# Performance work log

Hardware: AMD Instinct MI355X
Metric: run time of the kernel (lower is better)

Reference implementation:

```python
import jax, jax.numpy as jnp
import numpy as np


def setup_inputs() -> dict:
    key = jax.random.key(0)
    ks = jax.random.split(key, 6)
    B, S, T, E, D = 16, 128, 128, 512, 512  # batch, enc steps, dec steps, enc units, dec units
    scale = 0.05
    return {
        "enc": jax.random.normal(ks[0], (B, S, E), dtype=jnp.float32),
        "dec": jax.random.normal(ks[1], (B, T, D), dtype=jnp.float32),
        "W1": jax.random.normal(ks[2], (E, E), dtype=jnp.float32) * scale,
        "W2": jax.random.normal(ks[3], (D, E), dtype=jnp.float32) * scale,
        "b": jax.random.normal(ks[4], (1, 1, E), dtype=jnp.float32) * scale,
        "V": jax.random.normal(ks[5], (E, 1), dtype=jnp.float32) * scale,
    }


def reference(enc, dec, W1, W2, b, V):
    # Vectorized Bahdanau additive attention (the original loops over decoder
    # timesteps with keras.backend.rnn; the steps are independent so we batch them).
    W1_hs = jnp.einsum('bse,ef->bsf', enc, W1)            # [B,S,E] (computed once, not per step)
    W2_ht = jnp.einsum('btd,de->bte', dec, W2)            # [B,T,E]
    # tanh(W1.hs + W2.ht + b): broadcast to [B,T,S,E]
    scores = jnp.tanh(W1_hs[:, None, :, :] + W2_ht[:, :, None, :] + b)
    logits = jnp.einsum('btse,e->bts', scores, V[:, 0])   # [B,T,S]
    attn_weights = jax.nn.softmax(logits, axis=-1)        # softmax over encoder steps
    context_vectors = jnp.einsum('bts,bse->bte', attn_weights, enc)  # [B,T,E]
    return (context_vectors, attn_weights)
```

## Files before the change

### kernel.cpp

```cpp
#include <hip/hip_runtime.h>
#include <hip/hip_bf16.h>
#include <cstddef>


constexpr int nBt = 16, nSq = 128, nTq = 128, nEd = 512;

typedef __attribute__((ext_vector_type(4))) float f32x4;
typedef __attribute__((ext_vector_type(8))) short s16x8;

#define PRESCALE 2.8853900817779268f
#define LOG2E 1.4426950408889634f

__device__ __forceinline__ unsigned short to_bf(float f) {
    unsigned u = __builtin_bit_cast(unsigned, f);
    return (unsigned short)((u + 0x7FFFu + ((u >> 16) & 1u)) >> 16);
}
__device__ __forceinline__ float from_bf(unsigned short h) {
    unsigned u = ((unsigned)h) << 16;
    return __builtin_bit_cast(float, u);
}

__global__ __launch_bounds__(256) void kWprep(
    const float* __restrict__ W1, const float* __restrict__ W2,
    unsigned short* __restrict__ WT)
{
    const int z = blockIdx.z;
    const float* W = z ? W2 : W1;
    __shared__ float tl[32][33];
    const int r  = threadIdx.x >> 3;
    const int c4 = (threadIdx.x & 7) * 4;
    const int kB = blockIdx.y * 32;
    const int nB = blockIdx.x * 32;
    const float4 v = *(const float4*)&W[(size_t)(kB + r) * nEd + nB + c4];
    tl[r][c4 + 0] = v.x; tl[r][c4 + 1] = v.y;
    tl[r][c4 + 2] = v.z; tl[r][c4 + 3] = v.w;
    __syncthreads();
    unsigned short hh[4], ll[4];
    #pragma unroll
    for (int i = 0; i < 4; ++i) {
        const float x = tl[c4 + i][r];
        hh[i] = to_bf(x);
        ll[i] = to_bf(x - from_bf(hh[i]));
    }
    const size_t o = ((size_t)z * nEd + nB + r) * nEd + kB + c4;
    *(ushort4*)&WT[o] = *(ushort4*)hh;
    *(ushort4*)&WT[(size_t)2 * nEd * nEd + o] = *(ushort4*)ll;
}

__global__ __launch_bounds__(256) void kMgemm(
    const float* __restrict__ A0, const float* __restrict__ A1,
    const unsigned short* __restrict__ WT, const float* __restrict__ bias,
    float* __restrict__ C0, float* __restrict__ C1)
{
    const int z = blockIdx.z;
    const float* __restrict__ A = z ? A1 : A0;
    const unsigned short* __restrict__ Wh = WT + (size_t)z * nEd * nEd;
    const unsigned short* __restrict__ Wl = Wh + (size_t)2 * nEd * nEd;
    float* __restrict__ C = z ? C1 : C0;

    __shared__ unsigned short sAh[64][72];
    __shared__ unsigned short sAl[64][72];
    __shared__ unsigned short sBh[64][72];
    __shared__ unsigned short sBl[64][72];

    const int tid  = threadIdx.x;
    const int lane = tid & 63;
    const int wv   = tid >> 6;
    const int wm = (wv >> 1) * 32;
    const int wn = (wv & 1) * 32;
    const int rowB = blockIdx.y * 64;
    const int colB = blockIdx.x * 64;

    const int ar = tid >> 2, ak = (tid & 3) * 16;
    const int wr = tid >> 2, wk = (tid & 3) * 16;

    f32x4 acc[2][2] = {};
    const int l15 = lane & 15;
    const int kh  = lane >> 4;

    for (int k0 = 0; k0 < nEd; k0 += 64) {
        float4 ga[4];
        #pragma unroll
        for (int j = 0; j < 4; ++j)
            ga[j] = *(const float4*)&A[(size_t)(rowB + ar) * nEd + k0 + ak + 4 * j];
        const size_t wo = (size_t)(colB + wr) * nEd + k0 + wk;
        const s16x8 gh0 = *(const s16x8*)&Wh[wo];
        const s16x8 gh1 = *(const s16x8*)&Wh[wo + 8];
        const s16x8 gl0 = *(const s16x8*)&Wl[wo];
        const s16x8 gl1 = *(const s16x8*)&Wl[wo + 8];

        __syncthreads();
        #pragma unroll
        for (int j = 0; j < 4; ++j) {
            const float a4[4] = {ga[j].x, ga[j].y, ga[j].z, ga[j].w};
            unsigned short h[4], l[4];
            #pragma unroll
            for (int i = 0; i < 4; ++i) {
                h[i] = to_bf(a4[i]);
                l[i] = to_bf(a4[i] - from_bf(h[i]));
            }
            *(ushort4*)&sAh[ar][ak + 4 * j] = *(ushort4*)h;
            *(ushort4*)&sAl[ar][ak + 4 * j] = *(ushort4*)l;
        }
        *(s16x8*)&sBh[wr][wk]     = gh0;
        *(s16x8*)&sBh[wr][wk + 8] = gh1;
        *(s16x8*)&sBl[wr][wk]     = gl0;
        *(s16x8*)&sBl[wr][wk + 8] = gl1;
        __syncthreads();

        #pragma unroll
        for (int kk = 0; kk < 2; ++kk) {
            s16x8 fAh[2], fAl[2], fBh[2], fBl[2];
            #pragma unroll
            for (int mi = 0; mi < 2; ++mi) {
                fAh[mi] = *(const s16x8*)&sAh[wm + mi * 16 + l15][kk * 32 + kh * 8];
                fAl[mi] = *(const s16x8*)&sAl[wm + mi * 16 + l15][kk * 32 + kh * 8];
            }
            #pragma unroll
            for (int ni = 0; ni < 2; ++ni) {
                fBh[ni] = *(const s16x8*)&sBh[wn + ni * 16 + l15][kk * 32 + kh * 8];
                fBl[ni] = *(const s16x8*)&sBl[wn + ni * 16 + l15][kk * 32 + kh * 8];
            }
            #pragma unroll
            for (int mi = 0; mi < 2; ++mi)
                #pragma unroll
                for (int ni = 0; ni < 2; ++ni) {
                    f32x4 a = acc[mi][ni];
                    a = __builtin_amdgcn_mfma_f32_16x16x32_bf16(fAh[mi], fBh[ni], a, 0, 0, 0);
                    a = __builtin_amdgcn_mfma_f32_16x16x32_bf16(fAl[mi], fBh[ni], a, 0, 0, 0);
                    a = __builtin_amdgcn_mfma_f32_16x16x32_bf16(fAh[mi], fBl[ni], a, 0, 0, 0);
                    acc[mi][ni] = a;
                }
        }
    }

    #pragma unroll
    for (int ni = 0; ni < 2; ++ni) {
        const int col = colB + wn + ni * 16 + l15;
        const float bval = z ? bias[col] : 0.0f;
        #pragma unroll
        for (int mi = 0; mi < 2; ++mi) {
            #pragma unroll
            for (int r = 0; r < 4; ++r) {
                const int row = rowB + wm + mi * 16 + kh * 4 + r;
                C[(size_t)row * nEd + col] =
                    __builtin_amdgcn_exp2f((acc[mi][ni][r] + bval) * PRESCALE);
            }
        }
    }
}

__global__ __launch_bounds__(256) void kLogits(
    const float* __restrict__ X1e,
    const float* __restrict__ X2e,
    const float* __restrict__ V,
    float* __restrict__ lg)
{
    const int sg = blockIdx.x, tg = blockIdx.y, b = blockIdx.z;
    const int tid  = threadIdx.x;
    const int lane = tid & 63;
    const int w    = tid >> 6;
    const int s0 = sg * 32 + w * 8;
    const int t0 = tg * 4;

    const float4* vp = (const float4*)V;
    const float4  v0 = vp[lane * 2], v1 = vp[lane * 2 + 1];
    const float4 n0 = make_float4(-2.f * v0.x, -2.f * v0.y, -2.f * v0.z, -2.f * v0.w);
    const float4 n1 = make_float4(-2.f * v1.x, -2.f * v1.y, -2.f * v1.z, -2.f * v1.w);
    const float vsum = v0.x + v0.y + v0.z + v0.w + v1.x + v1.y + v1.z + v1.w;

    float4 c0[4], c1[4];
    #pragma unroll
    for (int i = 0; i < 4; ++i) {
        const float4* xp = (const float4*)(X2e + ((size_t)b * nTq + t0 + i) * nEd);
        c0[i] = xp[lane * 2];
        c1[i] = xp[lane * 2 + 1];
    }

    for (int si = 0; si < 8; ++si) {
        const int s = s0 + si;
        const float4* ap = (const float4*)(X1e + ((size_t)b * nSq + s) * nEd);
        const float4 x0 = ap[lane * 2], x1 = ap[lane * 2 + 1];
        float acc[4];
        #pragma unroll
        for (int t = 0; t < 4; ++t) {
            float a = vsum;
            a += n0.x * __builtin_amdgcn_rcpf(x0.x * c0[t].x + 1.0f);
            a += n0.y * __builtin_amdgcn_rcpf(x0.y * c0[t].y + 1.0f);
            a += n0.z * __builtin_amdgcn_rcpf(x0.z * c0[t].z + 1.0f);
            a += n0.w * __builtin_amdgcn_rcpf(x0.w * c0[t].w + 1.0f);
            a += n1.x * __builtin_amdgcn_rcpf(x1.x * c1[t].x + 1.0f);
            a += n1.y * __builtin_amdgcn_rcpf(x1.y * c1[t].y + 1.0f);
            a += n1.z * __builtin_amdgcn_rcpf(x1.z * c1[t].z + 1.0f);
            a += n1.w * __builtin_amdgcn_rcpf(x1.w * c1[t].w + 1.0f);
            acc[t] = a;
        }
        #pragma unroll
        for (int t = 0; t < 4; ++t) {
            float a = acc[t];
            #pragma unroll
            for (int off = 32; off >= 1; off >>= 1)
                a += __shfl_xor(a, off);
            if (lane == 0)
                lg[((size_t)b * nTq + t0 + t) * nSq + s] = a;
        }
    }
}

__global__ __launch_bounds__(256) void kEncT(
    const float* __restrict__ enc, unsigned short* __restrict__ encT)
{
    const int b = blockIdx.z;
    __shared__ float tl[32][33];
    const int r  = threadIdx.x >> 3;
    const int c4 = (threadIdx.x & 7) * 4;
    const int sB = blockIdx.y * 32;
    const int eB = blockIdx.x * 32;
    const float4 v = *(const float4*)&enc[((size_t)b * nSq + sB + r) * nEd + eB + c4];
    tl[r][c4 + 0] = v.x; tl[r][c4 + 1] = v.y;
    tl[r][c4 + 2] = v.z; tl[r][c4 + 3] = v.w;
    __syncthreads();
    unsigned short o[4];
    #pragma unroll
    for (int i = 0; i < 4; ++i) o[i] = to_bf(tl[c4 + i][r]);
    *(ushort4*)&encT[((size_t)b * nEd + eB + r) * nSq + sB + c4] = *(ushort4*)o;
}

__global__ __launch_bounds__(256) void kSoft(
    float* __restrict__ attnw,
    unsigned short* __restrict__ attnbf)
{
    const int bt = blockIdx.x * 4 + (threadIdx.x >> 6);
    const int lane = threadIdx.x & 63;
    const float l0 = attnw[(size_t)bt * nSq + lane];
    const float l1 = attnw[(size_t)bt * nSq + lane + 64];
    float m = fmaxf(l0, l1);
    #pragma unroll
    for (int off = 32; off >= 1; off >>= 1)
        m = fmaxf(m, __shfl_xor(m, off));
    const float e0 = __builtin_amdgcn_exp2f((l0 - m) * LOG2E);
    const float e1 = __builtin_amdgcn_exp2f((l1 - m) * LOG2E);
    float sum = e0 + e1;
    #pragma unroll
    for (int off = 32; off >= 1; off >>= 1)
        sum += __shfl_xor(sum, off);
    const float inv = __builtin_amdgcn_rcpf(sum);
    const float w0 = e0 * inv, w1 = e1 * inv;
    attnw[(size_t)bt * nSq + lane]      = w0;
    attnw[(size_t)bt * nSq + lane + 64] = w1;
    attnbf[(size_t)bt * nSq + lane]      = to_bf(w0);
    attnbf[(size_t)bt * nSq + lane + 64] = to_bf(w1);
}

__global__ __launch_bounds__(256) void kCtxMM(
    const unsigned short* __restrict__ attnbf,
    const unsigned short* __restrict__ encT,
    float* __restrict__ ctx)
{
    const int b  = blockIdx.z;
    const int tB = blockIdx.y * 32;
    const int eB = blockIdx.x * 64;

    __shared__ unsigned short sA[32][136];
    __shared__ unsigned short sB[64][136];

    const int tid  = threadIdx.x;
    const int lane = tid & 63;
    const int w    = tid >> 6;
    const int wm = (w >> 1) * 16;
    const int wn = (w & 1) * 32;
    const int l15 = lane & 15;
    const int kh  = lane >> 4;

    {
        const int r = tid >> 3, c = (tid & 7) * 16;
        const size_t o = ((size_t)b * nTq + tB + r) * nSq + c;
        *(s16x8*)&sA[r][c]     = *(const s16x8*)&attnbf[o];
        *(s16x8*)&sA[r][c + 8] = *(const s16x8*)&attnbf[o + 8];
    }
    {
        const int r = tid >> 2, c = (tid & 3) * 32;
        const size_t o = ((size_t)b * nEd + eB + r) * nSq + c;
        *(s16x8*)&sB[r][c]      = *(const s16x8*)&encT[o];
        *(s16x8*)&sB[r][c + 8]  = *(const s16x8*)&encT[o + 8];
        *(s16x8*)&sB[r][c + 16] = *(const s16x8*)&encT[o + 16];
        *(s16x8*)&sB[r][c + 24] = *(const s16x8*)&encT[o + 24];
    }
    __syncthreads();

    f32x4 acc[2] = {};
    #pragma unroll
    for (int kk = 0; kk < 4; ++kk) {
        const s16x8 fA = *(const s16x8*)&sA[wm + l15][kk * 32 + kh * 8];
        #pragma unroll
        for (int ni = 0; ni < 2; ++ni) {
            const s16x8 fB = *(const s16x8*)&sB[wn + ni * 16 + l15][kk * 32 + kh * 8];
            acc[ni] = __builtin_amdgcn_mfma_f32_16x16x32_bf16(fA, fB, acc[ni], 0, 0, 0);
        }
    }

    #pragma unroll
    for (int ni = 0; ni < 2; ++ni) {
        const int e = eB + wn + ni * 16 + l15;
        #pragma unroll
        for (int r = 0; r < 4; ++r) {
            const int t = tB + wm + kh * 4 + r;
            ctx[((size_t)b * nTq + t) * nEd + e] = acc[ni][r];
        }
    }
}

extern "C" void kernel_launch(void* const* d_in, const int* in_sizes, int n_in,
                              void* d_out, int out_size, void* d_ws, size_t ws_size,
                              hipStream_t stream) {
    const float* enc = (const float*)d_in[0];
    const float* dec = (const float*)d_in[1];
    const float* W1  = (const float*)d_in[2];
    const float* W2  = (const float*)d_in[3];
    const float* bv  = (const float*)d_in[4];
    const float* V   = (const float*)d_in[5];

    float* ctx   = (float*)d_out;
    float* attnw = (float*)d_out + (size_t)nBt * nTq * nEd;

    unsigned short* WT = (unsigned short*)d_out;

    float* ws0 = (float*)d_ws;
    float* ws1 = ws0 + (size_t)nBt * nSq * nEd;
    unsigned short* encT   = (unsigned short*)d_ws;
    unsigned short* attnbf = (unsigned short*)((char*)d_ws + 2*1024*1024);

    kWprep<<<dim3(nEd / 32, nEd / 32, 2), dim3(256), 0, stream>>>(W1, W2, WT);
    kMgemm<<<dim3(nEd / 64, (nBt * nSq) / 64, 2), dim3(256), 0, stream>>>(
        enc, dec, WT, bv, ws0, ws1);
    kLogits<<<dim3(4, 32, nBt), dim3(256), 0, stream>>>(ws0, ws1, V, attnw);
    kEncT<<<dim3(nEd / 32, nSq / 32, nBt), dim3(256), 0, stream>>>(enc, encT);
    kSoft<<<dim3((nBt * nTq) / 4), dim3(256), 0, stream>>>(attnw, attnbf);
    kCtxMM<<<dim3(nEd / 64, nTq / 32, nBt), dim3(256), 0, stream>>>(
        attnbf, encT, ctx);
}
```

Measured before the change: 59.40 us.

## Fuse logits with softmax, retile projection GEMM, convert attention weights in ctx GEMM

Result: slower. 84.76 us (+42.7%).

```diff
diff --git a/kernel.cpp b/kernel.cpp
--- a/kernel.cpp
+++ b/kernel.cpp
@@ -47,7 +47,7 @@
     *(ushort4*)&WT[(size_t)2 * nEd * nEd + o] = *(ushort4*)ll;
 }
 
-__global__ __launch_bounds__(256) void kMgemm(
+__global__ __launch_bounds__(256) void kMgemmB(
     const float* __restrict__ A0, const float* __restrict__ A1,
     const unsigned short* __restrict__ WT, const float* __restrict__ bias,
     float* __restrict__ C0, float* __restrict__ C1)
@@ -58,54 +58,55 @@
     const unsigned short* __restrict__ Wl = Wh + (size_t)2 * nEd * nEd;
     float* __restrict__ C = z ? C1 : C0;
 
-    __shared__ unsigned short sAh[64][72];
-    __shared__ unsigned short sAl[64][72];
-    __shared__ unsigned short sBh[64][72];
-    __shared__ unsigned short sBl[64][72];
+    __shared__ unsigned short sAh[32][72];
+    __shared__ unsigned short sAl[32][72];
+    __shared__ unsigned short sBh[128][72];
+    __shared__ unsigned short sBl[128][72];
 
     const int tid  = threadIdx.x;
     const int lane = tid & 63;
     const int wv   = tid >> 6;
-    const int wm = (wv >> 1) * 32;
-    const int wn = (wv & 1) * 32;
-    const int rowB = blockIdx.y * 64;
-    const int colB = blockIdx.x * 64;
-
-    const int ar = tid >> 2, ak = (tid & 3) * 16;
-    const int wr = tid >> 2, wk = (tid & 3) * 16;
+    const int rowB = blockIdx.y * 32;
+    const int colB = blockIdx.x * 128;
+
+    const int ar = tid >> 3, ak = (tid & 7) * 8;
+    const int br = tid >> 1, bc = (tid & 1) * 32;
 
     f32x4 acc[2][2] = {};
     const int l15 = lane & 15;
     const int kh  = lane >> 4;
 
     for (int k0 = 0; k0 < nEd; k0 += 64) {
-        float4 ga[4];
-        #pragma unroll
-        for (int j = 0; j < 4; ++j)
-            ga[j] = *(const float4*)&A[(size_t)(rowB + ar) * nEd + k0 + ak + 4 * j];
-        const size_t wo = (size_t)(colB + wr) * nEd + k0 + wk;
-        const s16x8 gh0 = *(const s16x8*)&Wh[wo];
-        const s16x8 gh1 = *(const s16x8*)&Wh[wo + 8];
-        const s16x8 gl0 = *(const s16x8*)&Wl[wo];
-        const s16x8 gl1 = *(const s16x8*)&Wl[wo + 8];
+        const float4 ga0 = *(const float4*)&A[(size_t)(rowB + ar) * nEd + k0 + ak];
+        const float4 ga1 = *(const float4*)&A[(size_t)(rowB + ar) * nEd + k0 + ak + 4];
+        const size_t wo = (size_t)(colB + br) * nEd + k0 + bc;
+        s16x8 gh[4], gl[4];
+        #pragma unroll
+        for (int j = 0; j < 4; ++j) {
+            gh[j] = *(const s16x8*)&Wh[wo + 8 * j];
+            gl[j] = *(const s16x8*)&Wl[wo + 8 * j];
+        }
 
         __syncthreads();
+        {
+            const float a8[8] = {ga0.x, ga0.y, ga0.z, ga0.w,
+                                 ga1.x, ga1.y, ga1.z, ga1.w};
+            unsigned short h[8], l[8];
+            #pragma unroll
+            for (int i = 0; i < 8; ++i) {
+                h[i] = to_bf(a8[i]);
+                l[i] = to_bf(a8[i] - from_bf(h[i]));
+            }
+            *(ushort4*)&sAh[ar][ak]     = *(ushort4*)&h[0];
+            *(ushort4*)&sAh[ar][ak + 4] = *(ushort4*)&h[4];
+            *(ushort4*)&sAl[ar][ak]     = *(ushort4*)&l[0];
+            *(ushort4*)&sAl[ar][ak + 4] = *(ushort4*)&l[4];
+        }
         #pragma unroll
         for (int j = 0; j < 4; ++j) {
-            const float a4[4] = {ga[j].x, ga[j].y, ga[j].z, ga[j].w};
-            unsigned short h[4], l[4];
-            #pragma unroll
-            for (int i = 0; i < 4; ++i) {
-                h[i] = to_bf(a4[i]);
-                l[i] = to_bf(a4[i] - from_bf(h[i]));
-            }
-            *(ushort4*)&sAh[ar][ak + 4 * j] = *(ushort4*)h;
-            *(ushort4*)&sAl[ar][ak + 4 * j] = *(ushort4*)l;
-        }
-        *(s16x8*)&sBh[wr][wk]     = gh0;
-        *(s16x8*)&sBh[wr][wk + 8] = gh1;
-        *(s16x8*)&sBl[wr][wk]     = gl0;
-        *(s16x8*)&sBl[wr][wk + 8] = gl1;
+            *(s16x8*)&sBh[br][bc + 8 * j] = gh[j];
+            *(s16x8*)&sBl[br][bc + 8 * j] = gl[j];
+        }
         __syncthreads();
 
         #pragma unroll
@@ -113,13 +114,13 @@
             s16x8 fAh[2], fAl[2], fBh[2], fBl[2];
             #pragma unroll
             for (int mi = 0; mi < 2; ++mi) {
-                fAh[mi] = *(const s16x8*)&sAh[wm + mi * 16 + l15][kk * 32 + kh * 8];
-                fAl[mi] = *(const s16x8*)&sAl[wm + mi * 16 + l15][kk * 32 + kh * 8];
+                fAh[mi] = *(const s16x8*)&sAh[mi * 16 + l15][kk * 32 + kh * 8];
+                fAl[mi] = *(const s16x8*)&sAl[mi * 16 + l15][kk * 32 + kh * 8];
             }
             #pragma unroll
             for (int ni = 0; ni < 2; ++ni) {
-                fBh[ni] = *(const s16x8*)&sBh[wn + ni * 16 + l15][kk * 32 + kh * 8];
-                fBl[ni] = *(const s16x8*)&sBl[wn + ni * 16 + l15][kk * 32 + kh * 8];
+                fBh[ni] = *(const s16x8*)&sBh[wv * 32 + ni * 16 + l15][kk * 32 + kh * 8];
+                fBl[ni] = *(const s16x8*)&sBl[wv * 32 + ni * 16 + l15][kk * 32 + kh * 8];
             }
             #pragma unroll
             for (int mi = 0; mi < 2; ++mi)
@@ -136,13 +137,13 @@
 
     #pragma unroll
     for (int ni = 0; ni < 2; ++ni) {
-        const int col = colB + wn + ni * 16 + l15;
+        const int col = colB + wv * 32 + ni * 16 + l15;
         const float bval = z ? bias[col] : 0.0f;
         #pragma unroll
         for (int mi = 0; mi < 2; ++mi) {
             #pragma unroll
             for (int r = 0; r < 4; ++r) {
-                const int row = rowB + wm + mi * 16 + kh * 4 + r;
+                const int row = rowB + mi * 16 + kh * 4 + r;
                 C[(size_t)row * nEd + col] =
                     __builtin_amdgcn_exp2f((acc[mi][ni][r] + bval) * PRESCALE);
             }
@@ -150,60 +151,97 @@
     }
 }
 
-__global__ __launch_bounds__(256) void kLogits(
+__global__ __launch_bounds__(256) void kLogSoft(
     const float* __restrict__ X1e,
     const float* __restrict__ X2e,
     const float* __restrict__ V,
-    float* __restrict__ lg)
-{
-    const int sg = blockIdx.x, tg = blockIdx.y, b = blockIdx.z;
+    float* __restrict__ attnw)
+{
+    const int tg = blockIdx.x, b = blockIdx.y;
     const int tid  = threadIdx.x;
     const int lane = tid & 63;
     const int w    = tid >> 6;
-    const int s0 = sg * 32 + w * 8;
     const int t0 = tg * 4;
 
-    const float4* vp = (const float4*)V;
-    const float4  v0 = vp[lane * 2], v1 = vp[lane * 2 + 1];
-    const float4 n0 = make_float4(-2.f * v0.x, -2.f * v0.y, -2.f * v0.z, -2.f * v0.w);
-    const float4 n1 = make_float4(-2.f * v1.x, -2.f * v1.y, -2.f * v1.z, -2.f * v1.w);
-    const float vsum = v0.x + v0.y + v0.z + v0.w + v1.x + v1.y + v1.z + v1.w;
-
-    float4 c0[4], c1[4];
-    #pragma unroll
-    for (int i = 0; i < 4; ++i) {
-        const float4* xp = (const float4*)(X2e + ((size_t)b * nTq + t0 + i) * nEd);
-        c0[i] = xp[lane * 2];
-        c1[i] = xp[lane * 2 + 1];
-    }
-
-    for (int si = 0; si < 8; ++si) {
-        const int s = s0 + si;
-        const float4* ap = (const float4*)(X1e + ((size_t)b * nSq + s) * nEd);
-        const float4 x0 = ap[lane * 2], x1 = ap[lane * 2 + 1];
-        float acc[4];
-        #pragma unroll
-        for (int t = 0; t < 4; ++t) {
-            float a = vsum;
-            a += n0.x * __builtin_amdgcn_rcpf(x0.x * c0[t].x + 1.0f);
-            a += n0.y * __builtin_amdgcn_rcpf(x0.y * c0[t].y + 1.0f);
-            a += n0.z * __builtin_amdgcn_rcpf(x0.z * c0[t].z + 1.0f);
-            a += n0.w * __builtin_amdgcn_rcpf(x0.w * c0[t].w + 1.0f);
-            a += n1.x * __builtin_amdgcn_rcpf(x1.x * c1[t].x + 1.0f);
-            a += n1.y * __builtin_amdgcn_rcpf(x1.y * c1[t].y + 1.0f);
-            a += n1.z * __builtin_amdgcn_rcpf(x1.z * c1[t].z + 1.0f);
-            a += n1.w * __builtin_amdgcn_rcpf(x1.w * c1[t].w + 1.0f);
-            acc[t] = a;
-        }
-        #pragma unroll
-        for (int t = 0; t < 4; ++t) {
-            float a = acc[t];
-            #pragma unroll
-            for (int off = 32; off >= 1; off >>= 1)
-                a += __shfl_xor(a, off);
-            if (lane == 0)
-                lg[((size_t)b * nTq + t0 + t) * nSq + s] = a;
-        }
+    __shared__ float x1t[128][68];
+    __shared__ float x2t[4][64];
+    __shared__ float nvt[64];
+    __shared__ float sm[4][nSq];
+
+    const int sr = 64 * (w & 1) + lane;
+    const int tp = (w >> 1) * 2;
+    const int srow = tid >> 1;
+    const int scol = (tid & 1) * 32;
+
+    const float* X1b = X1e + (size_t)b * nSq * nEd;
+    float acc0 = 0.f, acc1 = 0.f;
+
+    float4 pf[8];
+    #pragma unroll
+    for (int j = 0; j < 8; ++j)
+        pf[j] = *(const float4*)&X1b[(size_t)srow * nEd + scol + 4 * j];
+
+    for (int c = 0; c < 8; ++c) {
+        const int e0 = c * 64;
+        __syncthreads();
+        #pragma unroll
+        for (int j = 0; j < 8; ++j)
+            *(float4*)&x1t[srow][scol + 4 * j] = pf[j];
+        if (tid < 64) {
+            const int tt = tid >> 4, ee = (tid & 15) * 4;
+            *(float4*)&x2t[tt][ee] =
+                *(const float4*)&X2e[((size_t)b * nTq + t0 + tt) * nEd + e0 + ee];
+        } else if (tid < 80) {
+            const int ee = (tid - 64) * 4;
+            const float4 v = *(const float4*)&V[e0 + ee];
+            nvt[ee + 0] = -2.f * v.x; nvt[ee + 1] = -2.f * v.y;
+            nvt[ee + 2] = -2.f * v.z; nvt[ee + 3] = -2.f * v.w;
+        }
+        __syncthreads();
+
+        if (c < 7) {
+            #pragma unroll
+            for (int j = 0; j < 8; ++j)
+                pf[j] = *(const float4*)&X1b[(size_t)srow * nEd + e0 + 64 + scol + 4 * j];
+        }
+
+        #pragma unroll 4
+        for (int e4 = 0; e4 < 64; e4 += 4) {
+            const float4 x1v = *(const float4*)&x1t[sr][e4];
+            const float4 xa  = *(const float4*)&x2t[tp][e4];
+            const float4 xb  = *(const float4*)&x2t[tp + 1][e4];
+            const float4 nv  = *(const float4*)&nvt[e4];
+            acc0 += nv.x * __builtin_amdgcn_rcpf(x1v.x * xa.x + 1.0f);
+            acc1 += nv.x * __builtin_amdgcn_rcpf(x1v.x * xb.x + 1.0f);
+            acc0 += nv.y * __builtin_amdgcn_rcpf(x1v.y * xa.y + 1.0f);
+            acc1 += nv.y * __builtin_amdgcn_rcpf(x1v.y * xb.y + 1.0f);
+            acc0 += nv.z * __builtin_amdgcn_rcpf(x1v.z * xa.z + 1.0f);
+            acc1 += nv.z * __builtin_amdgcn_rcpf(x1v.z * xb.z + 1.0f);
+            acc0 += nv.w * __builtin_amdgcn_rcpf(x1v.w * xa.w + 1.0f);
+            acc1 += nv.w * __builtin_amdgcn_rcpf(x1v.w * xb.w + 1.0f);
+        }
+    }
+
+    sm[tp + 0][sr] = acc0;
+    sm[tp + 1][sr] = acc1;
+    __syncthreads();
+
+    {
+        const float l0 = sm[w][lane], l1 = sm[w][lane + 64];
+        float m = fmaxf(l0, l1);
+        #pragma unroll
+        for (int off = 32; off >= 1; off >>= 1)
+            m = fmaxf(m, __shfl_xor(m, off));
+        const float e0 = __builtin_amdgcn_exp2f((l0 - m) * LOG2E);
+        const float e1 = __builtin_amdgcn_exp2f((l1 - m) * LOG2E);
+        float sum = e0 + e1;
+        #pragma unroll
+        for (int off = 32; off >= 1; off >>= 1)
+            sum += __shfl_xor(sum, off);
+        const float inv = __builtin_amdgcn_rcpf(sum);
+        float* ap = attnw + ((size_t)b * nTq + t0 + w) * nSq;
+        ap[lane]      = e0 * inv;
+        ap[lane + 64] = e1 * inv;
     }
 }
 
@@ -226,34 +264,8 @@
     *(ushort4*)&encT[((size_t)b * nEd + eB + r) * nSq + sB + c4] = *(ushort4*)o;
 }
 
-__global__ __launch_bounds__(256) void kSoft(
-    float* __restrict__ attnw,
-    unsigned short* __restrict__ attnbf)
-{
-    const int bt = blockIdx.x * 4 + (threadIdx.x >> 6);
-    const int lane = threadIdx.x & 63;
-    const float l0 = attnw[(size_t)bt * nSq + lane];
-    const float l1 = attnw[(size_t)bt * nSq + lane + 64];
-    float m = fmaxf(l0, l1);
-    #pragma unroll
-    for (int off = 32; off >= 1; off >>= 1)
-        m = fmaxf(m, __shfl_xor(m, off));
-    const float e0 = __builtin_amdgcn_exp2f((l0 - m) * LOG2E);
-    const float e1 = __builtin_amdgcn_exp2f((l1 - m) * LOG2E);
-    float sum = e0 + e1;
-    #pragma unroll
-    for (int off = 32; off >= 1; off >>= 1)
-        sum += __shfl_xor(sum, off);
-    const float inv = __builtin_amdgcn_rcpf(sum);
-    const float w0 = e0 * inv, w1 = e1 * inv;
-    attnw[(size_t)bt * nSq + lane]      = w0;
-    attnw[(size_t)bt * nSq + lane + 64] = w1;
-    attnbf[(size_t)bt * nSq + lane]      = to_bf(w0);
-    attnbf[(size_t)bt * nSq + lane + 64] = to_bf(w1);
-}
-
 __global__ __launch_bounds__(256) void kCtxMM(
-    const unsigned short* __restrict__ attnbf,
+    const float* __restrict__ attnw,
     const unsigned short* __restrict__ encT,
     float* __restrict__ ctx)
 {
@@ -274,9 +286,16 @@
 
     {
         const int r = tid >> 3, c = (tid & 7) * 16;
-        const size_t o = ((size_t)b * nTq + tB + r) * nSq + c;
-        *(s16x8*)&sA[r][c]     = *(const s16x8*)&attnbf[o];
-        *(s16x8*)&sA[r][c + 8] = *(const s16x8*)&attnbf[o + 8];
+        const float* ap = &attnw[((size_t)b * nTq + tB + r) * nSq + c];
+        unsigned short h[16];
+        #pragma unroll
+        for (int q = 0; q < 4; ++q) {
+            const float4 v = *(const float4*)(ap + 4 * q);
+            h[4 * q + 0] = to_bf(v.x); h[4 * q + 1] = to_bf(v.y);
+            h[4 * q + 2] = to_bf(v.z); h[4 * q + 3] = to_bf(v.w);
+        }
+        *(s16x8*)&sA[r][c]     = *(s16x8*)&h[0];
+        *(s16x8*)&sA[r][c + 8] = *(s16x8*)&h[8];
     }
     {
         const int r = tid >> 2, c = (tid & 3) * 32;
@@ -327,15 +346,13 @@
 
     float* ws0 = (float*)d_ws;
     float* ws1 = ws0 + (size_t)nBt * nSq * nEd;
-    unsigned short* encT   = (unsigned short*)d_ws;
-    unsigned short* attnbf = (unsigned short*)((char*)d_ws + 2*1024*1024);
+    unsigned short* encT = (unsigned short*)d_ws;
 
     kWprep<<<dim3(nEd / 32, nEd / 32, 2), dim3(256), 0, stream>>>(W1, W2, WT);
-    kMgemm<<<dim3(nEd / 64, (nBt * nSq) / 64, 2), dim3(256), 0, stream>>>(
+    kMgemmB<<<dim3(nEd / 128, (nBt * nSq) / 32, 2), dim3(256), 0, stream>>>(
         enc, dec, WT, bv, ws0, ws1);
-    kLogits<<<dim3(4, 32, nBt), dim3(256), 0, stream>>>(ws0, ws1, V, attnw);
+    kLogSoft<<<dim3(nTq / 4, nBt), dim3(256), 0, stream>>>(ws0, ws1, V, attnw);
     kEncT<<<dim3(nEd / 32, nSq / 32, nBt), dim3(256), 0, stream>>>(enc, encT);
-    kSoft<<<dim3((nBt * nTq) / 4), dim3(256), 0, stream>>>(attnw, attnbf);
     kCtxMM<<<dim3(nEd / 64, nTq / 32, nBt), dim3(256), 0, stream>>>(
-        attnbf, encT, ctx);
-}
+        attnw, encT, ctx);
+}
```

## Reshape projection GEMM tiles and double decoder-step blocking in logits kernel

Applied to the files above, without the earlier changes.

Result: slower. 60.99 us (+2.7%).

```diff
diff --git a/kernel.cpp b/kernel.cpp
--- a/kernel.cpp
+++ b/kernel.cpp
@@ -47,7 +47,7 @@
     *(ushort4*)&WT[(size_t)2 * nEd * nEd + o] = *(ushort4*)ll;
 }
 
-__global__ __launch_bounds__(256) void kMgemm(
+__global__ __launch_bounds__(256) void kMgemmB(
     const float* __restrict__ A0, const float* __restrict__ A1,
     const unsigned short* __restrict__ WT, const float* __restrict__ bias,
     float* __restrict__ C0, float* __restrict__ C1)
@@ -58,54 +58,55 @@
     const unsigned short* __restrict__ Wl = Wh + (size_t)2 * nEd * nEd;
     float* __restrict__ C = z ? C1 : C0;
 
-    __shared__ unsigned short sAh[64][72];
-    __shared__ unsigned short sAl[64][72];
-    __shared__ unsigned short sBh[64][72];
-    __shared__ unsigned short sBl[64][72];
+    __shared__ unsigned short sAh[32][72];
+    __shared__ unsigned short sAl[32][72];
+    __shared__ unsigned short sBh[128][72];
+    __shared__ unsigned short sBl[128][72];
 
     const int tid  = threadIdx.x;
     const int lane = tid & 63;
     const int wv   = tid >> 6;
-    const int wm = (wv >> 1) * 32;
-    const int wn = (wv & 1) * 32;
-    const int rowB = blockIdx.y * 64;
-    const int colB = blockIdx.x * 64;
-
-    const int ar = tid >> 2, ak = (tid & 3) * 16;
-    const int wr = tid >> 2, wk = (tid & 3) * 16;
+    const int rowB = blockIdx.y * 32;
+    const int colB = blockIdx.x * 128;
+
+    const int ar = tid >> 3, ak = (tid & 7) * 8;
+    const int br = tid >> 1, bc = (tid & 1) * 32;
 
     f32x4 acc[2][2] = {};
     const int l15 = lane & 15;
     const int kh  = lane >> 4;
 
     for (int k0 = 0; k0 < nEd; k0 += 64) {
-        float4 ga[4];
-        #pragma unroll
-        for (int j = 0; j < 4; ++j)
-            ga[j] = *(const float4*)&A[(size_t)(rowB + ar) * nEd + k0 + ak + 4 * j];
-        const size_t wo = (size_t)(colB + wr) * nEd + k0 + wk;
-        const s16x8 gh0 = *(const s16x8*)&Wh[wo];
-        const s16x8 gh1 = *(const s16x8*)&Wh[wo + 8];
-        const s16x8 gl0 = *(const s16x8*)&Wl[wo];
-        const s16x8 gl1 = *(const s16x8*)&Wl[wo + 8];
+        const float4 ga0 = *(const float4*)&A[(size_t)(rowB + ar) * nEd + k0 + ak];
+        const float4 ga1 = *(const float4*)&A[(size_t)(rowB + ar) * nEd + k0 + ak + 4];
+        const size_t wo = (size_t)(colB + br) * nEd + k0 + bc;
+        s16x8 gh[4], gl[4];
+        #pragma unroll
+        for (int j = 0; j < 4; ++j) {
+            gh[j] = *(const s16x8*)&Wh[wo + 8 * j];
+            gl[j] = *(const s16x8*)&Wl[wo + 8 * j];
+        }
 
         __syncthreads();
+        {
+            const float a8[8] = {ga0.x, ga0.y, ga0.z, ga0.w,
+                                 ga1.x, ga1.y, ga1.z, ga1.w};
+            unsigned short h[8], l[8];
+            #pragma unroll
+            for (int i = 0; i < 8; ++i) {
+                h[i] = to_bf(a8[i]);
+                l[i] = to_bf(a8[i] - from_bf(h[i]));
+            }
+            *(ushort4*)&sAh[ar][ak]     = *(ushort4*)&h[0];
+            *(ushort4*)&sAh[ar][ak + 4] = *(ushort4*)&h[4];
+            *(ushort4*)&sAl[ar][ak]     = *(ushort4*)&l[0];
+            *(ushort4*)&sAl[ar][ak + 4] = *(ushort4*)&l[4];
+        }
         #pragma unroll
         for (int j = 0; j < 4; ++j) {
-            const float a4[4] = {ga[j].x, ga[j].y, ga[j].z, ga[j].w};
-            unsigned short h[4], l[4];
-            #pragma unroll
-            for (int i = 0; i < 4; ++i) {
-                h[i] = to_bf(a4[i]);
-                l[i] = to_bf(a4[i] - from_bf(h[i]));
-            }
-            *(ushort4*)&sAh[ar][ak + 4 * j] = *(ushort4*)h;
-            *(ushort4*)&sAl[ar][ak + 4 * j] = *(ushort4*)l;
-        }
-        *(s16x8*)&sBh[wr][wk]     = gh0;
-        *(s16x8*)&sBh[wr][wk + 8] = gh1;
-        *(s16x8*)&sBl[wr][wk]     = gl0;
-        *(s16x8*)&sBl[wr][wk + 8] = gl1;
+            *(s16x8*)&sBh[br][bc + 8 * j] = gh[j];
+            *(s16x8*)&sBl[br][bc + 8 * j] = gl[j];
+        }
         __syncthreads();
 
         #pragma unroll
@@ -113,13 +114,13 @@
             s16x8 fAh[2], fAl[2], fBh[2], fBl[2];
             #pragma unroll
             for (int mi = 0; mi < 2; ++mi) {
-                fAh[mi] = *(const s16x8*)&sAh[wm + mi * 16 + l15][kk * 32 + kh * 8];
-                fAl[mi] = *(const s16x8*)&sAl[wm + mi * 16 + l15][kk * 32 + kh * 8];
+                fAh[mi] = *(const s16x8*)&sAh[mi * 16 + l15][kk * 32 + kh * 8];
+                fAl[mi] = *(const s16x8*)&sAl[mi * 16 + l15][kk * 32 + kh * 8];
             }
             #pragma unroll
             for (int ni = 0; ni < 2; ++ni) {
-                fBh[ni] = *(const s16x8*)&sBh[wn + ni * 16 + l15][kk * 32 + kh * 8];
-                fBl[ni] = *(const s16x8*)&sBl[wn + ni * 16 + l15][kk * 32 + kh * 8];
+                fBh[ni] = *(const s16x8*)&sBh[wv * 32 + ni * 16 + l15][kk * 32 + kh * 8];
+                fBl[ni] = *(const s16x8*)&sBl[wv * 32 + ni * 16 + l15][kk * 32 + kh * 8];
             }
             #pragma unroll
             for (int mi = 0; mi < 2; ++mi)
@@ -136,13 +137,13 @@
 
     #pragma unroll
     for (int ni = 0; ni < 2; ++ni) {
-        const int col = colB + wn + ni * 16 + l15;
+        const int col = colB + wv * 32 + ni * 16 + l15;
         const float bval = z ? bias[col] : 0.0f;
         #pragma unroll
         for (int mi = 0; mi < 2; ++mi) {
             #pragma unroll
             for (int r = 0; r < 4; ++r) {
-                const int row = rowB + wm + mi * 16 + kh * 4 + r;
+                const int row = rowB + mi * 16 + kh * 4 + r;
                 C[(size_t)row * nEd + col] =
                     __builtin_amdgcn_exp2f((acc[mi][ni][r] + bval) * PRESCALE);
             }
@@ -161,17 +162,16 @@
     const int lane = tid & 63;
     const int w    = tid >> 6;
     const int s0 = sg * 32 + w * 8;
-    const int t0 = tg * 4;
+    const int t0 = tg * 8;
 
     const float4* vp = (const float4*)V;
     const float4  v0 = vp[lane * 2], v1 = vp[lane * 2 + 1];
     const float4 n0 = make_float4(-2.f * v0.x, -2.f * v0.y, -2.f * v0.z, -2.f * v0.w);
     const float4 n1 = make_float4(-2.f * v1.x, -2.f * v1.y, -2.f * v1.z, -2.f * v1.w);
-    const float vsum = v0.x + v0.y + v0.z + v0.w + v1.x + v1.y + v1.z + v1.w;
-
-    float4 c0[4], c1[4];
-    #pragma unroll
-    for (int i = 0; i < 4; ++i) {
+
+    float4 c0[8], c1[8];
+    #pragma unroll
+    for (int i = 0; i < 8; ++i) {
         const float4* xp = (const float4*)(X2e + ((size_t)b * nTq + t0 + i) * nEd);
         c0[i] = xp[lane * 2];
         c1[i] = xp[lane * 2 + 1];
@@ -181,22 +181,22 @@
         const int s = s0 + si;
         const float4* ap = (const float4*)(X1e + ((size_t)b * nSq + s) * nEd);
         const float4 x0 = ap[lane * 2], x1 = ap[lane * 2 + 1];
-        float acc[4];
-        #pragma unroll
-        for (int t = 0; t < 4; ++t) {
-            float a = vsum;
-            a += n0.x * __builtin_amdgcn_rcpf(x0.x * c0[t].x + 1.0f);
-            a += n0.y * __builtin_amdgcn_rcpf(x0.y * c0[t].y + 1.0f);
-            a += n0.z * __builtin_amdgcn_rcpf(x0.z * c0[t].z + 1.0f);
-            a += n0.w * __builtin_amdgcn_rcpf(x0.w * c0[t].w + 1.0f);
-            a += n1.x * __builtin_amdgcn_rcpf(x1.x * c1[t].x + 1.0f);
-            a += n1.y * __builtin_amdgcn_rcpf(x1.y * c1[t].y + 1.0f);
-            a += n1.z * __builtin_amdgcn_rcpf(x1.z * c1[t].z + 1.0f);
-            a += n1.w * __builtin_amdgcn_rcpf(x1.w * c1[t].w + 1.0f);
+        float acc[8];
+        #pragma unroll
+        for (int t = 0; t < 8; ++t) {
+            float a;
+            a  = n0.x * __builtin_amdgcn_rcpf(fmaf(x0.x, c0[t].x, 1.0f));
+            a += n0.y * __builtin_amdgcn_rcpf(fmaf(x0.y, c0[t].y, 1.0f));
+            a += n0.z * __builtin_amdgcn_rcpf(fmaf(x0.z, c0[t].z, 1.0f));
+            a += n0.w * __builtin_amdgcn_rcpf(fmaf(x0.w, c0[t].w, 1.0f));
+            a += n1.x * __builtin_amdgcn_rcpf(fmaf(x1.x, c1[t].x, 1.0f));
+            a += n1.y * __builtin_amdgcn_rcpf(fmaf(x1.y, c1[t].y, 1.0f));
+            a += n1.z * __builtin_amdgcn_rcpf(fmaf(x1.z, c1[t].z, 1.0f));
+            a += n1.w * __builtin_amdgcn_rcpf(fmaf(x1.w, c1[t].w, 1.0f));
             acc[t] = a;
         }
         #pragma unroll
-        for (int t = 0; t < 4; ++t) {
+        for (int t = 0; t < 8; ++t) {
             float a = acc[t];
             #pragma unroll
             for (int off = 32; off >= 1; off >>= 1)
@@ -331,9 +331,9 @@
     unsigned short* attnbf = (unsigned short*)((char*)d_ws + 2*1024*1024);
 
     kWprep<<<dim3(nEd / 32, nEd / 32, 2), dim3(256), 0, stream>>>(W1, W2, WT);
-    kMgemm<<<dim3(nEd / 64, (nBt * nSq) / 64, 2), dim3(256), 0, stream>>>(
+    kMgemmB<<<dim3(nEd / 128, (nBt * nSq) / 32, 2), dim3(256), 0, stream>>>(
         enc, dec, WT, bv, ws0, ws1);
-    kLogits<<<dim3(4, 32, nBt), dim3(256), 0, stream>>>(ws0, ws1, V, attnw);
+    kLogits<<<dim3(4, 16, nBt), dim3(256), 0, stream>>>(ws0, ws1, V, attnw);
     kEncT<<<dim3(nEd / 32, nSq / 32, nBt), dim3(256), 0, stream>>>(enc, encT);
     kSoft<<<dim3((nBt * nTq) / 4), dim3(256), 0, stream>>>(attnw, attnbf);
     kCtxMM<<<dim3(nEd / 64, nTq / 32, nBt), dim3(256), 0, stream>>>(
```
